# Optimization experiments

Hardware: AMD Instinct MI355X
Metric: run time of the kernel (lower is better)

## Reference

```python
import jax, jax.numpy as jnp
import numpy as np

B, T, D, H, QK, V, M = 2, 2048, 1024, 16, 64, 64, 1024
SOFTCAP = 50.0


def apply_rope(x, positions, max_wavelength=10000.0):
    # x: (B, T, H, d), positions: (T,)
    d = x.shape[-1]
    fraction = 2.0 * jnp.arange(d // 2, dtype=jnp.float32) / d
    timescale = max_wavelength ** fraction                      # (d/2,)
    sinusoid = positions.astype(jnp.float32)[:, None] / timescale  # (T, d/2)
    sin = jnp.sin(sinusoid)[:, None, :]  # (T, 1, d/2) broadcasts over heads
    cos = jnp.cos(sinusoid)[:, None, :]
    x1, x2 = jnp.split(x, 2, axis=-1)
    out = jnp.concatenate([x1 * cos - x2 * sin, x2 * cos + x1 * sin], axis=-1)
    return out.astype(x.dtype)


def rms_norm(x, scale, eps=1e-6):
    var = jnp.mean(jnp.square(x.astype(jnp.float32)), axis=-1, keepdims=True)
    normed = x * jax.lax.rsqrt(var + eps).astype(x.dtype)
    return normed * (1.0 + scale).astype(x.dtype)


def setup_inputs() -> dict:
    key = jax.random.key(0)
    ks = jax.random.split(key, 10)
    s = 0.02
    # key-padding mask: per-batch kv valid lengths (all rows have >=1536 valid keys)
    kv_lens = jnp.array([1536, 2048], dtype=jnp.int32)
    mask = (jnp.arange(T)[None, :] < kv_lens[:, None])  # (B, Tk)
    mask = jnp.broadcast_to(mask[:, None, None, :], (B, 1, T, T))
    return {
        "q": jax.random.normal(ks[0], (B, T, D), jnp.float32),
        "kv": jax.random.normal(ks[1], (B, T, D), jnp.float32),
        "mask": mask,
        "q_positions": jnp.arange(T, dtype=jnp.int32),
        "kv_positions": jnp.arange(T, dtype=jnp.int32),
        "wq": jax.random.normal(ks[2], (D, H * QK), jnp.float32) * s,
        "bq": jnp.zeros((H * QK,), jnp.float32),
        "wk": jax.random.normal(ks[3], (D, H * QK), jnp.float32) * s,
        "bk": jnp.zeros((H * QK,), jnp.float32),
        "wv": jax.random.normal(ks[4], (D, H * V), jnp.float32) * s,
        "bv": jnp.zeros((H * V,), jnp.float32),
        "q_scale": jnp.zeros((QK,), jnp.float32),
        "k_scale": jnp.zeros((QK,), jnp.float32),
        "wo": jax.random.normal(ks[5], (H * V, M), jnp.float32) * s,
        "bo": jnp.zeros((M,), jnp.float32),
    }


def reference(q, kv, mask, q_positions, kv_positions,
              wq, bq, wk, bk, wv, bv, q_scale, k_scale, wo, bo):
    qh = (q @ wq + bq).reshape(B, T, H, QK)
    kh = (kv @ wk + bk).reshape(B, T, H, QK)
    vh = (kv @ wv + bv).reshape(B, T, H, V)
    # QK RMSNorm
    qh = rms_norm(qh, q_scale)
    kh = rms_norm(kh, k_scale)
    # RoPE
    qh = apply_rope(qh, q_positions)
    kh = apply_rope(kh, kv_positions)
    # softcapped, masked attention
    logits = jnp.einsum("bthd,bThd->bhtT", qh, kh) / np.sqrt(QK).astype(jnp.float32)
    logits = SOFTCAP * jnp.tanh(logits / SOFTCAP)
    logits = jnp.where(mask, logits, -1e9)
    log_probs = jax.nn.log_softmax(logits, axis=-1)
    probs = jnp.exp(log_probs)
    probs = jnp.where(mask, probs, 0.0)
    # normalized attention entropy (B, H, T)
    entropy = -jnp.sum(probs * log_probs, axis=-1) / jnp.log(mask.sum(axis=-1))
    attn = jnp.einsum("bhtT,bThd->bthd", probs, vh).reshape(B, T, H * V)
    out = attn @ wo + bo
    return out, entropy
```

## Files before the change

kernel.cpp:

```cpp
#include <hip/hip_runtime.h>

#define BB 2
#define TT 2048
#define DD 1024
#define HH 16
#define QKD 64
#define VD 64
#define MD 1024

typedef _Float16 half4 __attribute__((ext_vector_type(4)));
typedef _Float16 half8 __attribute__((ext_vector_type(8)));
typedef __fp16 fp16x2 __attribute__((ext_vector_type(2)));
typedef float f32x4 __attribute__((ext_vector_type(4)));
typedef unsigned short us8 __attribute__((ext_vector_type(8)));
typedef unsigned short us4 __attribute__((ext_vector_type(4)));

__device__ __forceinline__ unsigned short f2h(float x){
    union { _Float16 h; unsigned short u; } c; c.h = (_Float16)x; return c.u;
}

__global__ __launch_bounds__(256) void k_cvt2(const float* __restrict__ a,
                                              const float* __restrict__ b,
                                              unsigned short* __restrict__ oa,
                                              unsigned short* __restrict__ ob){
    const int n = BB*TT*DD/4;
    int idx = blockIdx.x*256 + threadIdx.x;
    const float* src = (idx < n) ? a : b;
    unsigned short* dst = (idx < n) ? oa : ob;
    int i = ((idx < n) ? idx : idx - n)*4;
    const float4 v = *(const float4*)(src + i);
    us4 o; o.x = f2h(v.x); o.y = f2h(v.y); o.z = f2h(v.z); o.w = f2h(v.w);
    *(us4*)(dst + i) = o;
}

__global__ __launch_bounds__(256) void k_trw4(const float* __restrict__ w0,
                                              const float* __restrict__ w1,
                                              const float* __restrict__ w2,
                                              const float* __restrict__ w3,
                                              unsigned short* __restrict__ o0,
                                              unsigned short* __restrict__ o1,
                                              unsigned short* __restrict__ o2,
                                              unsigned short* __restrict__ o3){
    __shared__ float ts[64][65];
    int z = blockIdx.z;
    const float* in = (z==0) ? w0 : (z==1) ? w1 : (z==2) ? w2 : w3;
    unsigned short* out = (z==0) ? o0 : (z==1) ? o1 : (z==2) ? o2 : o3;
    int tid = threadIdx.x;
    int r0 = blockIdx.x*64, c0 = blockIdx.y*64;
    int lr = tid >> 4, lc = (tid & 15)*4;
#pragma unroll
    for (int i = 0; i < 4; ++i){
        const float4 v = *(const float4*)(in + (long)(r0 + lr + i*16)*1024 + c0 + lc);
        ts[lr+i*16][lc+0] = v.x; ts[lr+i*16][lc+1] = v.y;
        ts[lr+i*16][lc+2] = v.z; ts[lr+i*16][lc+3] = v.w;
    }
    __syncthreads();
    int oc = tid >> 2, rc = (tid & 3)*16;
    int ocp = oc;
    if (z < 2){
        int blk = oc >> 4;
        ocp = (blk == 1) ? oc + 16 : ((blk == 2) ? oc - 16 : oc);
    }
    us8 o0v, o1v;
#pragma unroll
    for (int j = 0; j < 8; ++j){ o0v[j] = f2h(ts[rc+j][ocp]); o1v[j] = f2h(ts[rc+8+j][ocp]); }
    *(us8*)(out + (long)(c0+oc)*1024 + r0 + rc)     = o0v;
    *(us8*)(out + (long)(c0+oc)*1024 + r0 + rc + 8) = o1v;
}

__global__ __launch_bounds__(256) void k_ropetab2(const int* __restrict__ qpos,
                                                  const int* __restrict__ kpos,
                                                  float* __restrict__ tabq,
                                                  float* __restrict__ tabk){
    int gi = blockIdx.x*256 + threadIdx.x;
    const int* pos = (gi < 65536) ? qpos : kpos;
    float* tab = (gi < 65536) ? tabq : tabk;
    int idx = gi & 65535;
    int t = idx >> 5, f = idx & 31;
    float invts = expf(-((float)f*(1.f/32.f)) * 9.210340371976184f);
    float ph = (float)pos[t]*invts;
    ((float2*)tab)[idx] = make_float2(sinf(ph), cosf(ph));
}

__global__ __launch_bounds__(256) void k_kvlen(const unsigned char* __restrict__ mask,
                                               int* __restrict__ kvlen){
    __shared__ int red[256];
    int b = blockIdx.x, tid = threadIdx.x;
    bool bytemode = (mask[1] != 0);
    int cnt = 0;
    for (int j = tid; j < TT; j += 256){
        long e = (long)b*TT*TT + j;
        if (bytemode) cnt += (mask[e] != 0);
        else          cnt += (((const unsigned int*)mask)[e] != 0);
    }
    red[tid] = cnt; __syncthreads();
    for (int s = 128; s > 0; s >>= 1){ if (tid < s) red[tid] += red[tid+s]; __syncthreads(); }
    if (tid == 0) kvlen[b] = red[0];
}

#define GEMM_CORE(A_, Bt_, abase, bbase)                                            \
    int rs = tid >> 3;                                                              \
    int cs = (tid & 7)*8;                                                           \
    int sws = (((tid & 7) ^ (rs & 7)))*16;                                          \
    int swb = lg ^ (li & 7);                                                        \
    us8 ra[4], rb[2];                                                               \
    _Pragma("unroll")                                                               \
    for (int c = 0; c < 4; ++c) ra[c] = *(const us8*)(A_  + (long)(m0 + rs + 32*c)*1024 + cs); \
    _Pragma("unroll")                                                               \
    for (int c = 0; c < 2; ++c) rb[c] = *(const us8*)(Bt_ + (long)(n0 + rs + 32*c)*1024 + cs); \
    _Pragma("unroll")                                                               \
    for (int c = 0; c < 4; ++c) *(us8*)(abase + (rs + 32*c)*128 + sws) = ra[c];     \
    _Pragma("unroll")                                                               \
    for (int c = 0; c < 2; ++c) *(us8*)(bbase + (rs + 32*c)*128 + sws) = rb[c];     \
    __syncthreads();                                                                \
    for (int ks = 0; ks < 16; ++ks){                                                \
        int cur = ks & 1;                                                           \
        bool pref = (ks + 1 < 16);                                                  \
        if (pref){                                                                  \
            int k0 = (ks + 1)*64;                                                   \
            _Pragma("unroll")                                                       \
            for (int c = 0; c < 4; ++c) ra[c] = *(const us8*)(A_  + (long)(m0 + rs + 32*c)*1024 + k0 + cs); \
            _Pragma("unroll")                                                       \
            for (int c = 0; c < 2; ++c) rb[c] = *(const us8*)(Bt_ + (long)(n0 + rs + 32*c)*1024 + k0 + cs); \
        }                                                                           \
        const char* ac = abase + cur*16384;                                         \
        const char* bc = bbase + cur*8192;                                          \
        _Pragma("unroll")                                                           \
        for (int kk = 0; kk < 2; ++kk){                                             \
            int co = ((kk*4) ^ swb)*16;                                             \
            half8 af[4], bf[2];                                                     \
            _Pragma("unroll")                                                       \
            for (int mi = 0; mi < 4; ++mi) af[mi] = *(const half8*)(ac + (wm + mi*16 + li)*128 + co); \
            _Pragma("unroll")                                                       \
            for (int ni = 0; ni < 2; ++ni) bf[ni] = *(const half8*)(bc + (wn + ni*16 + li)*128 + co); \
            _Pragma("unroll")                                                       \
            for (int mi = 0; mi < 4; ++mi)                                          \
                _Pragma("unroll")                                                   \
                for (int ni = 0; ni < 2; ++ni)                                      \
                    acc[mi][ni] = __builtin_amdgcn_mfma_f32_16x16x32_f16(af[mi], bf[ni], acc[mi][ni], 0, 0, 0); \
        }                                                                           \
        if (pref){                                                                  \
            char* an = abase + (cur^1)*16384;                                       \
            char* bn = bbase + (cur^1)*8192;                                        \
            _Pragma("unroll")                                                       \
            for (int c = 0; c < 4; ++c) *(us8*)(an + (rs + 32*c)*128 + sws) = ra[c];\
            _Pragma("unroll")                                                       \
            for (int c = 0; c < 2; ++c) *(us8*)(bn + (rs + 32*c)*128 + sws) = rb[c];\
        }                                                                           \
        __syncthreads();                                                            \
    }

__global__ __launch_bounds__(256) void k_gemm3(const unsigned short* __restrict__ q_bf,
                                               const unsigned short* __restrict__ kv_bf,
                                               const unsigned short* __restrict__ wqt,
                                               const unsigned short* __restrict__ wkt,
                                               const unsigned short* __restrict__ wvt,
                                               const float* __restrict__ bq,
                                               const float* __restrict__ bk,
                                               const float* __restrict__ bv,
                                               const float* __restrict__ qscale,
                                               const float* __restrict__ kscale,
                                               const float* __restrict__ tabq,
                                               const float* __restrict__ tabk,
                                               unsigned short* __restrict__ Qr,
                                               unsigned short* __restrict__ Kr,
                                               unsigned short* __restrict__ VTb){
    __shared__ float4 smem_[3072];
    char* abase = (char*)smem_;
    char* bbase = abase + 32768;
    int flat = blockIdx.x;
    int virt = (flat & 7)*192 + (flat >> 3);
    int z = virt >> 9;
    int rem = virt & 511;
    int m0 = (rem >> 4)*128;
    int nx = rem & 15;
    int n0 = nx*64;
    const unsigned short* A  = (z == 0) ? q_bf : kv_bf;
    const unsigned short* Bt = (z == 0) ? wqt : (z == 1) ? wkt : wvt;

    int tid = threadIdx.x, l = tid & 63, w = tid >> 6;
    int lg = l >> 4, li = l & 15;
    int wm = (w >> 1)*64, wn = (w & 1)*32;
    f32x4 zero = {0.f,0.f,0.f,0.f};
    f32x4 acc[4][2];
#pragma unroll
    for (int mi = 0; mi < 4; ++mi){ acc[mi][0] = zero; acc[mi][1] = zero; }
    GEMM_CORE(A, Bt, abase, bbase)

    int hd = nx;
    if (z < 2){
        const float* bias  = (z == 0) ? bq : bk;
        const float* scale = (z == 0) ? qscale : kscale;
        const float* tab   = (z == 0) ? tabq : tabk;
        unsigned short* out = (z == 0) ? Qr : Kr;
        float* hs = (float*)smem_;
        int d0 = (wn >> 1) + li;
        float b0 = bias[hd*64 + d0];
        float b1 = bias[hd*64 + d0 + 32];
        float ssp[4][4];
#pragma unroll
        for (int mi = 0; mi < 4; ++mi)
#pragma unroll
            for (int r = 0; r < 4; ++r){
                float x0 = acc[mi][0][r] + b0;
                float x1 = acc[mi][1][r] + b1;
                ssp[mi][r] = x0*x0 + x1*x1;
            }
#pragma unroll
        for (int m = 1; m < 16; m <<= 1)
#pragma unroll
            for (int mi = 0; mi < 4; ++mi)
#pragma unroll
                for (int r = 0; r < 4; ++r) ssp[mi][r] += __shfl_xor(ssp[mi][r], m);
        if (li == 0){
#pragma unroll
            for (int mi = 0; mi < 4; ++mi)
#pragma unroll
                for (int r = 0; r < 4; ++r)
                    hs[(wm + mi*16 + lg*4 + r)*2 + (w & 1)] = ssp[mi][r];
        }
        __syncthreads();
        float sc0 = 1.f + scale[d0];
        float sc1 = 1.f + scale[d0 + 32];
#pragma unroll
        for (int mi = 0; mi < 4; ++mi)
#pragma unroll
            for (int r = 0; r < 4; ++r){
                int row = wm + mi*16 + lg*4 + r;
                float ss = hs[row*2] + hs[row*2 + 1];
                float rstd = rsqrtf(ss*(1.f/64.f) + 1e-6f);
                float x0 = (acc[mi][0][r] + b0)*rstd*sc0;
                float x1 = (acc[mi][1][r] + b1)*rstd*sc1;
                int gm = m0 + row;
                int bb = gm >> 11, t = gm & 2047;
                float2 scv = ((const float2*)tab)[t*32 + d0];
                float o0 = x0*scv.y - x1*scv.x;
                float o1 = x1*scv.y + x0*scv.x;
                long obase = ((long)(bb*HH + hd)*TT + t)*64;
                out[obase + d0]      = f2h(o0);
                out[obase + d0 + 32] = f2h(o1);
            }
    } else {
        float* Tt = (float*)smem_;
#pragma unroll
        for (int mi = 0; mi < 4; ++mi)
#pragma unroll
            for (int ni = 0; ni < 2; ++ni){
                int col = wn + ni*16 + li;
                float bb = bv[hd*64 + col];
#pragma unroll
                for (int r = 0; r < 4; ++r)
                    Tt[col*133 + wm + mi*16 + lg*4 + r] = acc[mi][ni][r] + bb;
            }
        __syncthreads();
        int bb2 = m0 >> 11, t0 = m0 & 2047;
        int vd = tid >> 2, sg = (tid & 3)*32;
        long ob = ((long)(bb2*HH + hd)*64 + vd)*TT + t0 + sg;
#pragma unroll
        for (int c = 0; c < 4; ++c){
            us8 o;
#pragma unroll
            for (int j = 0; j < 8; ++j) o[j] = f2h(Tt[vd*133 + sg + c*8 + j]);
            *(us8*)(VTb + ob + c*8) = o;
        }
    }
}

__global__ __launch_bounds__(256) void k_gemm(const unsigned short* __restrict__ A,
                                              const unsigned short* __restrict__ Bt,
                                              const float* __restrict__ bias,
                                              float* __restrict__ C, int N){
    __shared__ float4 smem_[3072];
    char* abase = (char*)smem_;
    char* bbase = abase + 32768;
    int flat = blockIdx.x;
    int virt = (flat & 7)*64 + (flat >> 3);
    int m0 = (virt >> 4)*128, n0 = (virt & 15)*64;
    int tid = threadIdx.x, l = tid & 63, w = tid >> 6;
    int lg = l >> 4, li = l & 15;
    int wm = (w >> 1)*64, wn = (w & 1)*32;
    f32x4 zero = {0.f,0.f,0.f,0.f};
    f32x4 acc[4][2];
#pragma unroll
    for (int mi = 0; mi < 4; ++mi){ acc[mi][0] = zero; acc[mi][1] = zero; }
    GEMM_CORE(A, Bt, abase, bbase)
#pragma unroll
    for (int mi = 0; mi < 4; ++mi){
#pragma unroll
        for (int ni = 0; ni < 2; ++ni){
            int row = m0 + wm + mi*16 + lg*4;
            int col = n0 + wn + ni*16 + li;
            float bb = bias[col];
#pragma unroll
            for (int r = 0; r < 4; ++r)
                C[(long)(row + r)*N + col] = acc[mi][ni][r] + bb;
        }
    }
}

__global__ __launch_bounds__(512) void k_attn(const unsigned short* __restrict__ Qr,
                                              const unsigned short* __restrict__ Kr,
                                              const unsigned short* __restrict__ VT,
                                              const int* __restrict__ kvlen,
                                              unsigned short* __restrict__ attnb,
                                              float* __restrict__ ent){
    __shared__ unsigned short Ks[2][64][64];
    __shared__ unsigned short Vs[2][64][64];
    int tid = threadIdx.x;
    int l = tid & 63, w = tid >> 6;
    int lg = l >> 4, li = l & 15;
    int flat = blockIdx.x;
    int xcd = flat & 7;
    int idx = flat >> 3;
    int qt = idx & 15;
    int g = idx >> 4;
    int bh = xcd*2 + (g & 1) + (g >> 1)*16;
    int b = bh >> 4, h = bh & 15;
    long qk0 = (long)bh * TT * 64;
    long vt0 = (long)bh * 64 * TT;
    int kvl = kvlen[b];
    int q0 = qt*128 + w*16;

    half8 qf[2];
#pragma unroll
    for (int kk = 0; kk < 2; ++kk)
        qf[kk] = *(const half8*)(Qr + qk0 + (long)(q0 + li)*64 + kk*32 + lg*8);

    int r0s = tid >> 3;
    int kcs = (tid & 7)*8;
    int sws = (((tid & 7) ^ (r0s & 7)))*16;
    char* ksb = (char*)Ks;
    char* vsb = (char*)Vs;
    int swb = (lg >> 1) ^ (li & 7);
    int off8 = (lg & 1)*8;

    {
        us8 ka = *(const us8*)(Kr + qk0 + (long)r0s*64 + kcs);
        us8 va = *(const us8*)(VT + vt0 + (long)r0s*TT + kcs);
        *(us8*)(ksb + r0s*128 + sws) = ka;
        *(us8*)(vsb + r0s*128 + sws) = va;
    }
    __syncthreads();

    f32x4 zero = {0.f,0.f,0.f,0.f};
    f32x4 oacc[4];
#pragma unroll
    for (int jv = 0; jv < 4; ++jv) oacc[jv] = zero;
    float l_r = 0.f, s1_r = 0.f;

    const float PA = 0.18033688f;
    const float PB = -3.7570183e-7f;
    const float PC = 9.3925458e-13f;

    int nkv = (kvl + 63) >> 6;
    for (int kt = 0; kt < nkv; ++kt){
        int cur = kt & 1;
        const char* kc = ksb + cur*8192;
        const char* vc = vsb + cur*8192;
        us8 ka, va;
        bool pref = (kt + 1 < nkv);
        if (pref){
            int k0n = (kt+1)*64;
            ka = *(const us8*)(Kr + qk0 + (long)(k0n + r0s)*64 + kcs);
            va = *(const us8*)(VT + vt0 + (long)r0s*TT + k0n + kcs);
        }
        f32x4 sacc[4];
#pragma unroll
        for (int jt = 0; jt < 4; ++jt) sacc[jt] = zero;
#pragma unroll
        for (int kk = 0; kk < 2; ++kk){
            int co = ((kk*4 + lg) ^ (li & 7))*16;
#pragma unroll
            for (int jt = 0; jt < 4; ++jt){
                half8 kf = *(const half8*)(kc + (jt*16 + li)*128 + co);
                sacc[jt] = __builtin_amdgcn_mfma_f32_16x16x32_f16(kf, qf[kk], sacc[jt], 0, 0, 0);
            }
        }
        float xs2[4][4];
        bool tail = (kt*64 + 64 > kvl);
        if (tail){
#pragma unroll
            for (int jt = 0; jt < 4; ++jt){
#pragma unroll
                for (int r = 0; r < 4; ++r){
                    float u = sacc[jt][r];
                    float z2 = u*u;
                    float v = u*(PA + z2*(PB + z2*PC));
                    xs2[jt][r] = (kt*64 + jt*16 + lg*4 + r < kvl) ? v : -1e30f;
                }
            }
        } else {
#pragma unroll
            for (int jt = 0; jt < 4; ++jt){
#pragma unroll
                for (int r = 0; r < 4; ++r){
                    float u = sacc[jt][r];
                    float z2 = u*u;
                    xs2[jt][r] = u*(PA + z2*(PB + z2*PC));
                }
            }
        }
        float p[4][4];
#pragma unroll
        for (int jt = 0; jt < 4; ++jt){
#pragma unroll
            for (int r = 0; r < 4; ++r){
                float pp = exp2f(xs2[jt][r]);
                p[jt][r] = pp;
                l_r  += pp;
                s1_r += pp * xs2[jt][r];
            }
        }
        half4 pa[4];
#pragma unroll
        for (int kk = 0; kk < 4; ++kk){
            union { half4 v; fp16x2 h2[2]; } up;
            up.h2[0] = __builtin_amdgcn_cvt_pkrtz(p[kk][0], p[kk][1]);
            up.h2[1] = __builtin_amdgcn_cvt_pkrtz(p[kk][2], p[kk][3]);
            pa[kk] = up.v;
        }
#pragma unroll
        for (int kk = 0; kk < 4; ++kk){
            int co = (((kk*2) ^ swb))*16 + off8;
#pragma unroll
            for (int jv = 0; jv < 4; ++jv){
                half4 vf = *(const half4*)(vc + (jv*16 + li)*128 + co);
                oacc[jv] = __builtin_amdgcn_mfma_f32_16x16x16f16(pa[kk], vf, oacc[jv], 0, 0, 0);
            }
        }
        if (pref){
            int nb = (kt+1) & 1;
            *(us8*)(ksb + nb*8192 + r0s*128 + sws) = ka;
            *(us8*)(vsb + nb*8192 + r0s*128 + sws) = va;
        }
        __syncthreads();
    }

    l_r  += __shfl_xor(l_r, 16);  l_r  += __shfl_xor(l_r, 32);
    s1_r += __shfl_xor(s1_r, 16); s1_r += __shfl_xor(s1_r, 32);

    float invl = 1.f / l_r;
    float invr[4];
#pragma unroll
    for (int r = 0; r < 4; ++r) invr[r] = __shfl(invl, lg*4 + r);
#pragma unroll
    for (int jv = 0; jv < 4; ++jv){
#pragma unroll
        for (int r = 0; r < 4; ++r){
            int qrow = q0 + lg*4 + r;
            attnb[((long)b*TT + qrow)*1024 + h*64 + jv*16 + li] = f2h(oacc[jv][r]*invr[r]);
        }
    }
    if (l < 16){
        const float LN2 = 0.6931471805599453f;
        float lse = logf(l_r);
        float s1n = s1_r*LN2;
        ent[(long)bh*TT + q0 + li] = (lse - s1n*invl) / logf((float)kvl);
    }
}

extern "C" void kernel_launch(void* const* d_in, const int* in_sizes, int n_in,
                              void* d_out, int out_size, void* d_ws, size_t ws_size,
                              hipStream_t stream){
    (void)in_sizes; (void)n_in; (void)out_size; (void)ws_size;
    const float* q      = (const float*)d_in[0];
    const float* kv     = (const float*)d_in[1];
    const unsigned char* mask = (const unsigned char*)d_in[2];
    const int*   qpos   = (const int*)d_in[3];
    const int*   kpos   = (const int*)d_in[4];
    const float* wq     = (const float*)d_in[5];
    const float* bq     = (const float*)d_in[6];
    const float* wk     = (const float*)d_in[7];
    const float* bk     = (const float*)d_in[8];
    const float* wv     = (const float*)d_in[9];
    const float* bv     = (const float*)d_in[10];
    const float* qscale = (const float*)d_in[11];
    const float* kscale = (const float*)d_in[12];
    const float* wo     = (const float*)d_in[13];
    const float* bo     = (const float*)d_in[14];
    float* out = (float*)d_out;
    float* ent = out + (long)BB*TT*MD;

    char* ws = (char*)d_ws;
    unsigned short* wqt   = (unsigned short*)(ws);
    unsigned short* wkt   = (unsigned short*)(ws + 2097152L);
    unsigned short* wvt   = (unsigned short*)(ws + 4194304L);
    unsigned short* wot   = (unsigned short*)(ws + 6291456L);
    unsigned short* q_bf  = (unsigned short*)(ws + 8388608L);
    unsigned short* kv_bf = (unsigned short*)(ws + 16777216L);
    unsigned short* Qr    = (unsigned short*)(ws + 25165824L);
    unsigned short* Kr    = (unsigned short*)(ws + 33554432L);
    unsigned short* VTb   = (unsigned short*)(ws + 41943040L);
    unsigned short* attnb = (unsigned short*)(ws + 50331648L);
    float*          tabq  = (float*)(ws + 58720256L);
    float*          tabk  = (float*)(ws + 59244544L);
    int*            kvln  = (int*)(ws + 59768832L);

    k_cvt2<<<8192, 256, 0, stream>>>(q, kv, q_bf, kv_bf);
    k_trw4<<<dim3(16,16,4), 256, 0, stream>>>(wq, wk, wv, wo, wqt, wkt, wvt, wot);
    k_ropetab2<<<512, 256, 0, stream>>>(qpos, kpos, tabq, tabk);
    k_kvlen<<<2, 256, 0, stream>>>(mask, kvln);

    k_gemm3<<<1536, 256, 0, stream>>>(q_bf, kv_bf, wqt, wkt, wvt,
                                      bq, bk, bv, qscale, kscale,
                                      tabq, tabk, Qr, Kr, VTb);

    k_attn<<<512, 512, 0, stream>>>(Qr, Kr, VTb, kvln, attnb, ent);

    k_gemm<<<512, 256, 0, stream>>>(attnb, wot, bo, out, 1024);
}
```

Before: 154.1 us.

## Merge prep kernels into one launch and process two KV tiles per attention stage

The four preprocessing kernels (input fp16 conversion, weight transpose, RoPE table, kv-length count) are folded into one launch that dispatches on block index, cutting three kernel launches and the gaps between them. The attention kernel now double-buffers pairs of 64-key tiles (128 keys per stage), which halves the number of barrier syncs and issues more global loads per prefetch. In exchange LDS use per block doubles, which can lower occupancy, and the larger prefetch holds more registers live.

```diff
diff --git a/kernel.cpp b/kernel.cpp
--- a/kernel.cpp
+++ b/kernel.cpp
@@ -19,83 +19,85 @@
     union { _Float16 h; unsigned short u; } c; c.h = (_Float16)x; return c.u;
 }
 
-__global__ __launch_bounds__(256) void k_cvt2(const float* __restrict__ a,
-                                              const float* __restrict__ b,
-                                              unsigned short* __restrict__ oa,
-                                              unsigned short* __restrict__ ob){
-    const int n = BB*TT*DD/4;
-    int idx = blockIdx.x*256 + threadIdx.x;
-    const float* src = (idx < n) ? a : b;
-    unsigned short* dst = (idx < n) ? oa : ob;
-    int i = ((idx < n) ? idx : idx - n)*4;
-    const float4 v = *(const float4*)(src + i);
-    us4 o; o.x = f2h(v.x); o.y = f2h(v.y); o.z = f2h(v.z); o.w = f2h(v.w);
-    *(us4*)(dst + i) = o;
-}
-
-__global__ __launch_bounds__(256) void k_trw4(const float* __restrict__ w0,
+__global__ __launch_bounds__(256) void k_prep(const float* __restrict__ q,
+                                              const float* __restrict__ kv,
+                                              unsigned short* __restrict__ q_bf,
+                                              unsigned short* __restrict__ kv_bf,
+                                              const float* __restrict__ w0,
                                               const float* __restrict__ w1,
                                               const float* __restrict__ w2,
                                               const float* __restrict__ w3,
                                               unsigned short* __restrict__ o0,
                                               unsigned short* __restrict__ o1,
                                               unsigned short* __restrict__ o2,
-                                              unsigned short* __restrict__ o3){
-    __shared__ float ts[64][65];
-    int z = blockIdx.z;
-    const float* in = (z==0) ? w0 : (z==1) ? w1 : (z==2) ? w2 : w3;
-    unsigned short* out = (z==0) ? o0 : (z==1) ? o1 : (z==2) ? o2 : o3;
-    int tid = threadIdx.x;
-    int r0 = blockIdx.x*64, c0 = blockIdx.y*64;
-    int lr = tid >> 4, lc = (tid & 15)*4;
-#pragma unroll
-    for (int i = 0; i < 4; ++i){
-        const float4 v = *(const float4*)(in + (long)(r0 + lr + i*16)*1024 + c0 + lc);
-        ts[lr+i*16][lc+0] = v.x; ts[lr+i*16][lc+1] = v.y;
-        ts[lr+i*16][lc+2] = v.z; ts[lr+i*16][lc+3] = v.w;
-    }
-    __syncthreads();
-    int oc = tid >> 2, rc = (tid & 3)*16;
-    int ocp = oc;
-    if (z < 2){
-        int blk = oc >> 4;
-        ocp = (blk == 1) ? oc + 16 : ((blk == 2) ? oc - 16 : oc);
-    }
-    us8 o0v, o1v;
-#pragma unroll
-    for (int j = 0; j < 8; ++j){ o0v[j] = f2h(ts[rc+j][ocp]); o1v[j] = f2h(ts[rc+8+j][ocp]); }
-    *(us8*)(out + (long)(c0+oc)*1024 + r0 + rc)     = o0v;
-    *(us8*)(out + (long)(c0+oc)*1024 + r0 + rc + 8) = o1v;
-}
-
-__global__ __launch_bounds__(256) void k_ropetab2(const int* __restrict__ qpos,
-                                                  const int* __restrict__ kpos,
-                                                  float* __restrict__ tabq,
-                                                  float* __restrict__ tabk){
-    int gi = blockIdx.x*256 + threadIdx.x;
-    const int* pos = (gi < 65536) ? qpos : kpos;
-    float* tab = (gi < 65536) ? tabq : tabk;
-    int idx = gi & 65535;
-    int t = idx >> 5, f = idx & 31;
-    float invts = expf(-((float)f*(1.f/32.f)) * 9.210340371976184f);
-    float ph = (float)pos[t]*invts;
-    ((float2*)tab)[idx] = make_float2(sinf(ph), cosf(ph));
-}
-
-__global__ __launch_bounds__(256) void k_kvlen(const unsigned char* __restrict__ mask,
-                                               int* __restrict__ kvlen){
-    __shared__ int red[256];
-    int b = blockIdx.x, tid = threadIdx.x;
-    bool bytemode = (mask[1] != 0);
-    int cnt = 0;
-    for (int j = tid; j < TT; j += 256){
-        long e = (long)b*TT*TT + j;
-        if (bytemode) cnt += (mask[e] != 0);
-        else          cnt += (((const unsigned int*)mask)[e] != 0);
-    }
-    red[tid] = cnt; __syncthreads();
-    for (int s = 128; s > 0; s >>= 1){ if (tid < s) red[tid] += red[tid+s]; __syncthreads(); }
-    if (tid == 0) kvlen[b] = red[0];
+                                              unsigned short* __restrict__ o3,
+                                              const int* __restrict__ qpos,
+                                              const int* __restrict__ kpos,
+                                              float* __restrict__ tabq,
+                                              float* __restrict__ tabk,
+                                              const unsigned char* __restrict__ mask,
+                                              int* __restrict__ kvlen){
+    __shared__ float smem[64*65];
+    int bid = blockIdx.x, tid = threadIdx.x;
+    if (bid < 8192){
+        const int n = BB*TT*DD/4;
+        int idx = bid*256 + tid;
+        const float* src = (idx < n) ? q : kv;
+        unsigned short* dst = (idx < n) ? q_bf : kv_bf;
+        int i = ((idx < n) ? idx : idx - n)*4;
+        const float4 v = *(const float4*)(src + i);
+        us4 o; o.x = f2h(v.x); o.y = f2h(v.y); o.z = f2h(v.z); o.w = f2h(v.w);
+        *(us4*)(dst + i) = o;
+    } else if (bid < 9216){
+        int idx2 = bid - 8192;
+        int z = idx2 >> 8;
+        int rc2 = idx2 & 255;
+        const float* in = (z==0) ? w0 : (z==1) ? w1 : (z==2) ? w2 : w3;
+        unsigned short* out = (z==0) ? o0 : (z==1) ? o1 : (z==2) ? o2 : o3;
+        float (*ts)[65] = (float(*)[65])smem;
+        int r0 = (rc2 & 15)*64, c0 = (rc2 >> 4)*64;
+        int lr = tid >> 4, lc = (tid & 15)*4;
+#pragma unroll
+        for (int i = 0; i < 4; ++i){
+            const float4 v = *(const float4*)(in + (long)(r0 + lr + i*16)*1024 + c0 + lc);
+            ts[lr+i*16][lc+0] = v.x; ts[lr+i*16][lc+1] = v.y;
+            ts[lr+i*16][lc+2] = v.z; ts[lr+i*16][lc+3] = v.w;
+        }
+        __syncthreads();
+        int oc = tid >> 2, rc = (tid & 3)*16;
+        int ocp = oc;
+        if (z < 2){
+            int blk = oc >> 4;
+            ocp = (blk == 1) ? oc + 16 : ((blk == 2) ? oc - 16 : oc);
+        }
+        us8 o0v, o1v;
+#pragma unroll
+        for (int j = 0; j < 8; ++j){ o0v[j] = f2h(ts[rc+j][ocp]); o1v[j] = f2h(ts[rc+8+j][ocp]); }
+        *(us8*)(out + (long)(c0+oc)*1024 + r0 + rc)     = o0v;
+        *(us8*)(out + (long)(c0+oc)*1024 + r0 + rc + 8) = o1v;
+    } else if (bid < 9728){
+        int gi = (bid - 9216)*256 + tid;
+        const int* pos = (gi < 65536) ? qpos : kpos;
+        float* tab = (gi < 65536) ? tabq : tabk;
+        int idx = gi & 65535;
+        int t = idx >> 5, f = idx & 31;
+        float invts = expf(-((float)f*(1.f/32.f)) * 9.210340371976184f);
+        float ph = (float)pos[t]*invts;
+        ((float2*)tab)[idx] = make_float2(sinf(ph), cosf(ph));
+    } else {
+        int* red = (int*)smem;
+        int b = bid - 9728;
+        bool bytemode = (mask[1] != 0);
+        int cnt = 0;
+        for (int j = tid; j < TT; j += 256){
+            long e = (long)b*TT*TT + j;
+            if (bytemode) cnt += (mask[e] != 0);
+            else          cnt += (((const unsigned int*)mask)[e] != 0);
+        }
+        red[tid] = cnt; __syncthreads();
+        for (int s = 128; s > 0; s >>= 1){ if (tid < s) red[tid] += red[tid+s]; __syncthreads(); }
+        if (tid == 0) kvlen[b] = red[0];
+    }
 }
 
 #define GEMM_CORE(A_, Bt_, abase, bbase)                                            \
@@ -304,8 +306,8 @@
                                               const int* __restrict__ kvlen,
                                               unsigned short* __restrict__ attnb,
                                               float* __restrict__ ent){
-    __shared__ unsigned short Ks[2][64][64];
-    __shared__ unsigned short Vs[2][64][64];
+    __shared__ unsigned short Ks[2][128][64];
+    __shared__ unsigned short Vs[2][64][128];
     int tid = threadIdx.x;
     int l = tid & 63, w = tid >> 6;
     int lg = l >> 4, li = l & 15;
@@ -334,11 +336,20 @@
     int swb = (lg >> 1) ^ (li & 7);
     int off8 = (lg & 1)*8;
 
+    int nkv = (kvl + 63) >> 6;
+    int npair = (nkv + 1) >> 1;
+
     {
-        us8 ka = *(const us8*)(Kr + qk0 + (long)r0s*64 + kcs);
-        us8 va = *(const us8*)(VT + vt0 + (long)r0s*TT + kcs);
-        *(us8*)(ksb + r0s*128 + sws) = ka;
-        *(us8*)(vsb + r0s*128 + sws) = va;
+        us8 ka0 = *(const us8*)(Kr + qk0 + (long)r0s*64 + kcs);
+        *(us8*)(ksb + r0s*128 + sws) = ka0;
+        us8 va0 = *(const us8*)(VT + vt0 + (long)r0s*TT + kcs);
+        *(us8*)(vsb + r0s*256 + sws) = va0;
+        if (1 < nkv){
+            us8 ka1 = *(const us8*)(Kr + qk0 + (long)(64 + r0s)*64 + kcs);
+            *(us8*)(ksb + (64 + r0s)*128 + sws) = ka1;
+            us8 va1 = *(const us8*)(VT + vt0 + (long)r0s*TT + 64 + kcs);
+            *(us8*)(vsb + r0s*256 + sws + 128) = va1;
+        }
     }
     __syncthreads();
 
@@ -352,86 +363,102 @@
     const float PB = -3.7570183e-7f;
     const float PC = 9.3925458e-13f;
 
-    int nkv = (kvl + 63) >> 6;
-    for (int kt = 0; kt < nkv; ++kt){
-        int cur = kt & 1;
-        const char* kc = ksb + cur*8192;
-        const char* vc = vsb + cur*8192;
-        us8 ka, va;
-        bool pref = (kt + 1 < nkv);
-        if (pref){
-            int k0n = (kt+1)*64;
-            ka = *(const us8*)(Kr + qk0 + (long)(k0n + r0s)*64 + kcs);
-            va = *(const us8*)(VT + vt0 + (long)r0s*TT + k0n + kcs);
-        }
-        f32x4 sacc[4];
-#pragma unroll
-        for (int jt = 0; jt < 4; ++jt) sacc[jt] = zero;
-#pragma unroll
-        for (int kk = 0; kk < 2; ++kk){
-            int co = ((kk*4 + lg) ^ (li & 7))*16;
-#pragma unroll
-            for (int jt = 0; jt < 4; ++jt){
-                half8 kf = *(const half8*)(kc + (jt*16 + li)*128 + co);
-                sacc[jt] = __builtin_amdgcn_mfma_f32_16x16x32_f16(kf, qf[kk], sacc[jt], 0, 0, 0);
-            }
-        }
-        float xs2[4][4];
-        bool tail = (kt*64 + 64 > kvl);
-        if (tail){
-#pragma unroll
-            for (int jt = 0; jt < 4; ++jt){
-#pragma unroll
-                for (int r = 0; r < 4; ++r){
-                    float u = sacc[jt][r];
-                    float z2 = u*u;
-                    float v = u*(PA + z2*(PB + z2*PC));
-                    xs2[jt][r] = (kt*64 + jt*16 + lg*4 + r < kvl) ? v : -1e30f;
+    for (int it = 0; it < npair; ++it){
+        int cur = it & 1;
+        const char* kc = ksb + cur*16384;
+        const char* vc = vsb + cur*16384;
+        us8 ka0, ka1, va0, va1;
+        int kt2 = (it + 1)*2;
+        bool pf0 = (kt2 < nkv), pf1 = (kt2 + 1 < nkv);
+        if (pf0){
+            int k0n = kt2*64;
+            ka0 = *(const us8*)(Kr + qk0 + (long)(k0n + r0s)*64 + kcs);
+            va0 = *(const us8*)(VT + vt0 + (long)r0s*TT + k0n + kcs);
+        }
+        if (pf1){
+            int k0n = kt2*64 + 64;
+            ka1 = *(const us8*)(Kr + qk0 + (long)(k0n + r0s)*64 + kcs);
+            va1 = *(const us8*)(VT + vt0 + (long)r0s*TT + k0n + kcs);
+        }
+#pragma unroll
+        for (int sub = 0; sub < 2; ++sub){
+            int kt = it*2 + sub;
+            if (kt < nkv){
+                f32x4 sacc[4];
+#pragma unroll
+                for (int jt = 0; jt < 4; ++jt) sacc[jt] = zero;
+#pragma unroll
+                for (int kk = 0; kk < 2; ++kk){
+                    int co = ((kk*4 + lg) ^ (li & 7))*16;
+#pragma unroll
+                    for (int jt = 0; jt < 4; ++jt){
+                        half8 kf = *(const half8*)(kc + (sub*64 + jt*16 + li)*128 + co);
+                        sacc[jt] = __builtin_amdgcn_mfma_f32_16x16x32_f16(kf, qf[kk], sacc[jt], 0, 0, 0);
+                    }
+                }
+                float xs2[4][4];
+                bool tail = (kt*64 + 64 > kvl);
+                if (tail){
+#pragma unroll
+                    for (int jt = 0; jt < 4; ++jt){
+#pragma unroll
+                        for (int r = 0; r < 4; ++r){
+                            float u = sacc[jt][r];
+                            float z2 = u*u;
+                            float v = u*(PA + z2*(PB + z2*PC));
+                            xs2[jt][r] = (kt*64 + jt*16 + lg*4 + r < kvl) ? v : -1e30f;
+                        }
+                    }
+                } else {
+#pragma unroll
+                    for (int jt = 0; jt < 4; ++jt){
+#pragma unroll
+                        for (int r = 0; r < 4; ++r){
+                            float u = sacc[jt][r];
+                            float z2 = u*u;
+                            xs2[jt][r] = u*(PA + z2*(PB + z2*PC));
+                        }
+                    }
+                }
+                float p[4][4];
+#pragma unroll
+                for (int jt = 0; jt < 4; ++jt){
+#pragma unroll
+                    for (int r = 0; r < 4; ++r){
+                        float pp = exp2f(xs2[jt][r]);
+                        p[jt][r] = pp;
+                        l_r  += pp;
+                        s1_r += pp * xs2[jt][r];
+                    }
+                }
+                half4 pa[4];
+#pragma unroll
+                for (int kk = 0; kk < 4; ++kk){
+                    union { half4 v; fp16x2 h2[2]; } up;
+                    up.h2[0] = __builtin_amdgcn_cvt_pkrtz(p[kk][0], p[kk][1]);
+                    up.h2[1] = __builtin_amdgcn_cvt_pkrtz(p[kk][2], p[kk][3]);
+                    pa[kk] = up.v;
+                }
+#pragma unroll
+                for (int kk = 0; kk < 4; ++kk){
+                    int co = sub*128 + ((kk*2) ^ swb)*16 + off8;
+#pragma unroll
+                    for (int jv = 0; jv < 4; ++jv){
+                        half4 vf = *(const half4*)(vc + (jv*16 + li)*256 + co);
+                        oacc[jv] = __builtin_amdgcn_mfma_f32_16x16x16f16(pa[kk], vf, oacc[jv], 0, 0, 0);
+                    }
                 }
             }
-        } else {
-#pragma unroll
-            for (int jt = 0; jt < 4; ++jt){
-#pragma unroll
-                for (int r = 0; r < 4; ++r){
-                    float u = sacc[jt][r];
-                    float z2 = u*u;
-                    xs2[jt][r] = u*(PA + z2*(PB + z2*PC));
-                }
+        }
+        if (pf0){
+            char* kn = ksb + (cur^1)*16384;
+            char* vn = vsb + (cur^1)*16384;
+            *(us8*)(kn + r0s*128 + sws) = ka0;
+            *(us8*)(vn + r0s*256 + sws) = va0;
+            if (pf1){
+                *(us8*)(kn + (64 + r0s)*128 + sws) = ka1;
+                *(us8*)(vn + r0s*256 + sws + 128) = va1;
             }
-        }
-        float p[4][4];
-#pragma unroll
-        for (int jt = 0; jt < 4; ++jt){
-#pragma unroll
-            for (int r = 0; r < 4; ++r){
-                float pp = exp2f(xs2[jt][r]);
-                p[jt][r] = pp;
-                l_r  += pp;
-                s1_r += pp * xs2[jt][r];
-            }
-        }
-        half4 pa[4];
-#pragma unroll
-        for (int kk = 0; kk < 4; ++kk){
-            union { half4 v; fp16x2 h2[2]; } up;
-            up.h2[0] = __builtin_amdgcn_cvt_pkrtz(p[kk][0], p[kk][1]);
-            up.h2[1] = __builtin_amdgcn_cvt_pkrtz(p[kk][2], p[kk][3]);
-            pa[kk] = up.v;
-        }
-#pragma unroll
-        for (int kk = 0; kk < 4; ++kk){
-            int co = (((kk*2) ^ swb))*16 + off8;
-#pragma unroll
-            for (int jv = 0; jv < 4; ++jv){
-                half4 vf = *(const half4*)(vc + (jv*16 + li)*128 + co);
-                oacc[jv] = __builtin_amdgcn_mfma_f32_16x16x16f16(pa[kk], vf, oacc[jv], 0, 0, 0);
-            }
-        }
-        if (pref){
-            int nb = (kt+1) & 1;
-            *(us8*)(ksb + nb*8192 + r0s*128 + sws) = ka;
-            *(us8*)(vsb + nb*8192 + r0s*128 + sws) = va;
         }
         __syncthreads();
     }
@@ -496,10 +523,9 @@
     float*          tabk  = (float*)(ws + 59244544L);
     int*            kvln  = (int*)(ws + 59768832L);
 
-    k_cvt2<<<8192, 256, 0, stream>>>(q, kv, q_bf, kv_bf);
-    k_trw4<<<dim3(16,16,4), 256, 0, stream>>>(wq, wk, wv, wo, wqt, wkt, wvt, wot);
-    k_ropetab2<<<512, 256, 0, stream>>>(qpos, kpos, tabq, tabk);
-    k_kvlen<<<2, 256, 0, stream>>>(mask, kvln);
+    k_prep<<<9730, 256, 0, stream>>>(q, kv, q_bf, kv_bf,
+                                     wq, wk, wv, wo, wqt, wkt, wvt, wot,
+                                     qpos, kpos, tabq, tabk, mask, kvln);
 
     k_gemm3<<<1536, 256, 0, stream>>>(q_bf, kv_bf, wqt, wkt, wvt,
                                       bq, bk, bv, qscale, kscale,
```

Measured after the change: 147.6 us. -4.2%, faster.
